# Optimization experiments

Measured on AMD Instinct MI355X. Metric: run time of the kernel, lower is better.

## Reference

```python
import jax, jax.numpy as jnp
import numpy as np

T_OUT = 12  # num_timesteps_output


def setup_inputs() -> dict:
    key = jax.random.key(0)
    ks = jax.random.split(key, 12)
    B, N, T, F = 32, 325, 12, 2
    C, H = 10, 64
    s = 0.08  # weight init scale (~1/sqrt(H)) to keep gates in sane range
    return {
        "A": jnp.zeros((N, N), jnp.float32),
        "X": jax.random.normal(ks[0], (B, N, T, F), jnp.float32),
        "enc_Wih": jax.random.normal(ks[1], (C, 3 * H, F), jnp.float32) * s,
        "enc_Whh": jax.random.normal(ks[2], (C, 3 * H, H), jnp.float32) * s,
        "enc_bih": jax.random.normal(ks[3], (C, 3 * H), jnp.float32) * s,
        "enc_bhh": jax.random.normal(ks[4], (C, 3 * H), jnp.float32) * s,
        "dec_Wih": jax.random.normal(ks[5], (C, 3 * H, 1), jnp.float32) * s,
        "dec_Whh": jax.random.normal(ks[6], (C, 3 * H, H), jnp.float32) * s,
        "dec_bih": jax.random.normal(ks[7], (C, 3 * H), jnp.float32) * s,
        "dec_bhh": jax.random.normal(ks[8], (C, 3 * H), jnp.float32) * s,
        "lin_W": jax.random.normal(ks[9], (C, 1, H), jnp.float32) * s,
        "lin_b": jax.random.normal(ks[10], (C, 1), jnp.float32) * s,
        "embed": jax.random.normal(ks[11], (N, C), jnp.float32),
    }


def _gru_update(gi, gh, h, H):
    # PyTorch GRU gate order: r, z, n
    r = jax.nn.sigmoid(gi[..., :H] + gh[..., :H])
    z = jax.nn.sigmoid(gi[..., H:2 * H] + gh[..., H:2 * H])
    n = jnp.tanh(gi[..., 2 * H:] + r * gh[..., 2 * H:])
    return (1.0 - z) * n + z * h


def reference(A, X, enc_Wih, enc_Whh, enc_bih, enc_bhh,
              dec_Wih, dec_Whh, dec_bih, dec_bhh, lin_W, lin_b, embed):
    B, N, T, F = X.shape
    C = enc_Wih.shape[0]
    H = enc_Whh.shape[-1]
    BN = B * N

    # (T, BN, F): time-major, batch*nodes flattened (matches X.view(-1,T,F).permute(1,0,2))
    Xs = jnp.transpose(X.reshape(BN, T, F), (1, 0, 2))

    def enc_step(h, x_t):  # h: (C, BN, H), x_t: (BN, F)
        gi = jnp.einsum('bf,cgf->cbg', x_t, enc_Wih) + enc_bih[:, None, :]
        gh = jnp.einsum('cbh,cgh->cbg', h, enc_Whh) + enc_bhh[:, None, :]
        return _gru_update(gi, gh, h, H), None

    h0 = jnp.zeros((C, BN, H), X.dtype)
    h_enc, _ = jax.lax.scan(enc_step, h0, Xs)  # (C, BN, H)

    # initial decoder input: last observed value of feature 0
    lv0 = jnp.broadcast_to(Xs[-1, :, 0][None, :, None], (C, BN, 1))

    def dec_step(carry, _):
        h, lv = carry
        gi = jnp.einsum('cbf,cgf->cbg', lv, dec_Wih) + dec_bih[:, None, :]
        gh = jnp.einsum('cbh,cgh->cbg', h, dec_Whh) + dec_bhh[:, None, :]
        h = _gru_update(gi, gh, h, H)
        value = jnp.einsum('cbh,coh->cbo', h, lin_W) + lin_b[:, None, :]  # (C, BN, 1)
        # original does last_value = value.detach()
        return (h, jax.lax.stop_gradient(value)), value

    (_, _), vals = jax.lax.scan(dec_step, (h_enc, lv0), None, length=T_OUT)
    # vals: (T_out, C, BN, 1) -> (B, N, T_out, C)
    out = jnp.transpose(vals[..., 0], (2, 0, 1)).reshape(B, N, T_OUT, C)

    weight = jax.nn.softmax(embed, axis=-1)  # (N, C)
    return jnp.einsum('bntc,nc->bnt', out, weight)
```

## Files before the change

### kernel.cpp

```cpp
#include <hip/hip_runtime.h>
#include <math.h>

#define N_     325
#define BN_    10400
#define OUTSZ_ (BN_*12)
#define RB_    208
#define WV_    13
#define THR_   832


typedef _Float16 h8v  __attribute__((ext_vector_type(8)));
typedef float    f4v  __attribute__((ext_vector_type(4)));
typedef unsigned int u32x4 __attribute__((ext_vector_type(4)));

#define L1C 1.4426950408889634f
#define L2C 2.8853900817779268f

__device__ __forceinline__ float rcp_f(float x){ return __builtin_amdgcn_rcpf(x); }
#if __has_builtin(__builtin_amdgcn_exp2f)
__device__ __forceinline__ float exp2_f(float x){ return __builtin_amdgcn_exp2f(x); }
#else
__device__ __forceinline__ float exp2_f(float x){ return __expf(x * 0.6931471805599453f); }
#endif

__device__ __forceinline__ unsigned short f16u(float x){
    union { _Float16 h; unsigned short u; } cv; cv.h = (_Float16)x; return cv.u;
}

#define BOFF   0
#define EOFF   24576
#define HOFF   27648
#define XOFF   57600
#define WOFF   67584
#define LOFF   68416
#define SMEMSZ 69248

#define MFMA(A,B,C) __builtin_amdgcn_mfma_f32_16x16x32_f16((A),(B),(C),0,0,0)

__device__ __forceinline__ void stage_main(const float* __restrict__ W, char* smem, int tid)
{
#pragma unroll
    for (int it = 0; it < 2; ++it) {
        int a16 = it*THR_ + tid;
        if (a16 < 1536) {
            int f     = a16 >> 6;
            int lanew = a16 & 63;
            int colf  = lanew & 15;
            int kb4   = lanew >> 4;
            int ch    = f & 1;
            int ct    = (f >> 1) & 3;
            int g     = f >> 3;
            int gc    = g*64 + ct*16 + colf;
            int k0    = ch*32 + kb4*8;
            float sc  = (g < 2) ? -L1C : -L2C;
            const float* p = W + gc*64 + k0;
            float4 a = *(const float4*)p;
            float4 b = *(const float4*)(p+4);
            h8v v;
            v[0]=(_Float16)(sc*a.x); v[1]=(_Float16)(sc*a.y);
            v[2]=(_Float16)(sc*a.z); v[3]=(_Float16)(sc*a.w);
            v[4]=(_Float16)(sc*b.x); v[5]=(_Float16)(sc*b.y);
            v[6]=(_Float16)(sc*b.z); v[7]=(_Float16)(sc*b.w);
            *(h8v*)(smem + BOFF + a16*16) = v;
        }
    }
}

__device__ __forceinline__ void rnn_step(h8v Aeh, h8v Ah0, h8v Ah1,
                                         const char* bb, const char* eb,
                                         const float cbh[4], float (&hreg)[4][4],
                                         char* wp)
{
    const f4v Z0 = {0.f,0.f,0.f,0.f};
#pragma unroll
    for (int ct = 0; ct < 4; ++ct) {
        f4v a0 = MFMA(Aeh, *(const h8v*)(eb + ct*256),       Z0);
        a0 = MFMA(Ah0, *(const h8v*)(bb + (ct*2   )*1024), a0);
        a0 = MFMA(Ah1, *(const h8v*)(bb + (ct*2+1 )*1024), a0);
        f4v a1 = MFMA(Aeh, *(const h8v*)(eb + (4+ct)*256),   Z0);
        a1 = MFMA(Ah0, *(const h8v*)(bb + (8+ct*2 )*1024), a1);
        a1 = MFMA(Ah1, *(const h8v*)(bb + (9+ct*2 )*1024), a1);
        f4v a3 = MFMA(Aeh, *(const h8v*)(eb + (8+ct)*256),   Z0);
        f4v a2 = MFMA(Ah0, *(const h8v*)(bb + (16+ct*2)*1024), Z0);
        a2 = MFMA(Ah1, *(const h8v*)(bb + (17+ct*2)*1024), a2);
#pragma unroll
        for (int i = 0; i < 4; ++i) {
            float er = exp2_f(a0[i]);
            float rr = rcp_f(1.0f + er);
            float ez = exp2_f(a1[i]);
            float en = exp2_f(fmaf(rr, a2[i] + cbh[ct], a3[i]));
            float h  = hreg[ct][i];
            float aa = 1.0f + ez;
            float den = fmaf(en, aa, aa);
            float t1  = fmaf(-en, ez, ez);
            float t2  = fmaf(en, h, h);
            float hnew = (t1 + t2) * rcp_f(den);
            hreg[ct][i] = hnew;
            *(_Float16*)(wp + i*144 + 32*ct) = (_Float16)hnew;
        }
    }
}

__global__ void __launch_bounds__(THR_, 6) krnn_kernel(
    const float* __restrict__ X,
    const float* __restrict__ eWih, const float* __restrict__ eWhh,
    const float* __restrict__ ebih, const float* __restrict__ ebhh,
    const float* __restrict__ dWih, const float* __restrict__ dWhh,
    const float* __restrict__ dbih, const float* __restrict__ dbhh,
    const float* __restrict__ linW, const float* __restrict__ linb,
    const float* __restrict__ embed, float* __restrict__ ws)
{
    __shared__ __align__(16) char smem[SMEMSZ];

    const int c    = blockIdx.y;
    const int row0 = blockIdx.x * RB_;
    const int tid  = threadIdx.x;
    const int lane = tid & 63;
    const int w    = tid >> 6;
    const int l15  = lane & 15;
    const int kg   = lane >> 4;

    stage_main(eWhh + c*12288, smem, tid);

    if (tid < 192) {
        int e = tid >> 4, ln = tid & 15;
        int g = e >> 2, ct = e & 3;
        int gc = g*64 + ct*16 + ln;
        float sc = (g < 2) ? -L1C : -L2C;
        float w0 = eWih[c*384 + gc*2], w1 = eWih[c*384 + gc*2 + 1];
        float bb_ = (g < 2) ? (ebih[c*192+gc] + ebhh[c*192+gc]) : ebih[c*192+gc];
        unsigned short* d = (unsigned short*)(smem + EOFF + e*256 + ln*16);
        d[0] = f16u(sc*w0); d[1] = f16u(sc*w1); d[2] = f16u(sc*bb_);
        d[3]=0; d[4]=0; d[5]=0; d[6]=0; d[7]=0;
    }
    for (int i = tid; i < RB_*12; i += THR_) {
        int r = i / 12, t = i - r*12;
        int rg = row0 + r;
        const float* p = X + (size_t)rg*24 + t*2;
        unsigned v = (unsigned)f16u(p[0]) | ((unsigned)f16u(p[1]) << 16);
        *(unsigned*)(smem + XOFF + r*48 + t*4) = v;
    }
    if (tid < RB_) {
        int r = row0 + tid;
        int n = r % N_;
        float e[10], mx = -1e30f;
#pragma unroll
        for (int cc=0; cc<10; ++cc){ e[cc]=embed[n*10+cc]; mx=fmaxf(mx,e[cc]); }
        float den = 0.0f;
#pragma unroll
        for (int cc=0; cc<10; ++cc) den += exp2_f((e[cc]-mx)*L1C);
        *(float*)(smem + WOFF + tid*4) = exp2_f((e[c]-mx)*L1C) * rcp_f(den);
    }
    for (int i = tid; i < WV_*576; i += THR_)
        *(unsigned*)(smem + HOFF + i*4) = 0u;

    float cbh[4];
#pragma unroll
    for (int ct=0; ct<4; ++ct) cbh[ct] = -L2C * ebhh[c*192 + 128 + l15 + 16*ct];

    __syncthreads();

    float wreg[4];
#pragma unroll
    for (int i=0;i<4;++i) wreg[i] = *(const float*)(smem + WOFF + (w*16 + kg*4 + i)*4);

    char* hp = smem + HOFF + w*2304;
    const int rdo = l15*144 + kg*16;
    char* wp = hp + kg*576 + l15*2;
    const char* bb = smem + lane*16;
    const char* eb = smem + EOFF + l15*16;

    float hreg[4][4];
#pragma unroll
    for (int ct=0; ct<4; ++ct)
#pragma unroll
        for (int i=0;i<4;++i) hreg[ct][i] = 0.0f;

    for (int t = 0; t < 12; ++t) {
        unsigned xd = *(const unsigned*)(smem + XOFF + (w*16 + l15)*48 + t*4);
        union { u32x4 u; h8v h; } ae;
        ae.u.x = (lane < 16) ? xd : 0u;
        ae.u.y = (lane < 16) ? 0x00003C00u : 0u;
        ae.u.z = 0u; ae.u.w = 0u;
        h8v Ah0 = *(const h8v*)(hp + rdo);
        h8v Ah1 = *(const h8v*)(hp + rdo + 64);
        rnn_step(ae.h, Ah0, Ah1, bb, eb, cbh, hreg, wp);
    }

    unsigned aew = (*(const unsigned*)(smem + XOFF + (w*16 + l15)*48 + 44) & 0xFFFFu)
                   | 0x3C000000u;

    __syncthreads();

    stage_main(dWhh + c*12288, smem, tid);
    if (tid < 192) {
        int e = tid >> 4, ln = tid & 15;
        int g = e >> 2, ct = e & 3;
        int gc = g*64 + ct*16 + ln;
        float k0, k1;
        if (g < 2) { k0 = -L1C*dWih[c*192+gc]; k1 = -L1C*(dbih[c*192+gc]+dbhh[c*192+gc]); }
        else       { k0 = -L2C*dWih[c*192+gc]; k1 = -L2C*dbih[c*192+gc]; }
        unsigned short* d = (unsigned short*)(smem + EOFF + e*256 + ln*16);
        d[0] = f16u(k0); d[1] = f16u(k1);
        d[2]=0; d[3]=0; d[4]=0; d[5]=0; d[6]=0; d[7]=0;
    }
    h8v Blw[2];
#pragma unroll
    for (int ch=0; ch<2; ++ch) {
        const float* p = linW + c*64 + ch*32 + kg*8;
        float4 a = *(const float4*)p;
        float4 b = *(const float4*)(p+4);
        h8v v;
        v[0]=(_Float16)a.x; v[1]=(_Float16)a.y; v[2]=(_Float16)a.z; v[3]=(_Float16)a.w;
        v[4]=(_Float16)b.x; v[5]=(_Float16)b.y; v[6]=(_Float16)b.z; v[7]=(_Float16)b.w;
        Blw[ch] = v;
    }
#pragma unroll
    for (int ct=0; ct<4; ++ct) cbh[ct] = -L2C * dbhh[c*192 + 128 + l15 + 16*ct];
    const float lb = linb[c];
    float* __restrict__ wsc = ws + (size_t)c * OUTSZ_;

    __syncthreads();

    for (int s = 0; s < 12; ++s) {
        h8v Ah0 = *(const h8v*)(hp + rdo);
        h8v Ah1 = *(const h8v*)(hp + rdo + 64);
        if (s > 0) {
            const f4v Zv = {0.f,0.f,0.f,0.f};
            f4v av = MFMA(Ah0, Blw[0], Zv);
            av = MFMA(Ah1, Blw[1], av);
            if (l15 == 0) {
#pragma unroll
                for (int i=0;i<4;++i) {
                    float lv = av[i] + lb;
                    *(float*)(smem + LOFF + w*64 + (kg*4+i)*4) = lv;
                    int r = row0 + w*16 + kg*4 + i;
                    wsc[(size_t)r*12 + (s-1)] = wreg[i]*lv;
                }
            }
            float lvme = *(const float*)(smem + LOFF + w*64 + l15*4);
            aew = (unsigned)f16u(lvme) | 0x3C000000u;
        }
        union { u32x4 u; h8v h; } ae;
        ae.u.x = (lane < 16) ? aew : 0u;
        ae.u.y = 0u; ae.u.z = 0u; ae.u.w = 0u;
        rnn_step(ae.h, Ah0, Ah1, bb, eb, cbh, hreg, wp);
    }

    {
        h8v Ah0 = *(const h8v*)(hp + rdo);
        h8v Ah1 = *(const h8v*)(hp + rdo + 64);
        const f4v Zv = {0.f,0.f,0.f,0.f};
        f4v av = MFMA(Ah0, Blw[0], Zv);
        av = MFMA(Ah1, Blw[1], av);
        if (l15 == 0) {
#pragma unroll
            for (int i=0;i<4;++i) {
                float lv = av[i] + lb;
                int r = row0 + w*16 + kg*4 + i;
                wsc[(size_t)r*12 + 11] = wreg[i]*lv;
            }
        }
    }
}

__global__ void __launch_bounds__(256) mix_kernel(const float* __restrict__ ws,
                                                  float* __restrict__ out)
{
    int i = blockIdx.x * 256 + threadIdx.x;
    if (i < OUTSZ_) {
        float s = 0.0f;
#pragma unroll
        for (int c = 0; c < 10; ++c) s += ws[(size_t)c * OUTSZ_ + i];
        out[i] = s;
    }
}

extern "C" void kernel_launch(void* const* d_in, const int* in_sizes, int n_in,
                              void* d_out, int out_size, void* d_ws, size_t ws_size,
                              hipStream_t stream) {
    const float* X    = (const float*)d_in[1];
    const float* eWih = (const float*)d_in[2];
    const float* eWhh = (const float*)d_in[3];
    const float* ebih = (const float*)d_in[4];
    const float* ebhh = (const float*)d_in[5];
    const float* dWih = (const float*)d_in[6];
    const float* dWhh = (const float*)d_in[7];
    const float* dbih = (const float*)d_in[8];
    const float* dbhh = (const float*)d_in[9];
    const float* linW = (const float*)d_in[10];
    const float* linb = (const float*)d_in[11];
    const float* emb  = (const float*)d_in[12];
    float* ws  = (float*)d_ws;
    float* out = (float*)d_out;

    dim3 grid(BN_ / RB_, 10);
    krnn_kernel<<<grid, dim3(THR_), 0, stream>>>(
        X, eWih, eWhh, ebih, ebhh, dWih, dWhh, dbih, dbhh, linW, linb, emb, ws);
    mix_kernel<<<(OUTSZ_ + 255) / 256, dim3(256), 0, stream>>>(ws, out);
}
```

Measured before the change: 228.6 us.

## Move decoder linear weights and softmax weights to LDS to cut registers

Stores the fp16 decoder output-projection weights in shared memory, and reads the per-row softmax mixing weights from shared memory at use instead of keeping both in registers. Adds a scheduling barrier after each gate tile in the RNN step and raises the launch-bounds occupancy hint from 6 to 8 waves. The aim is lower VGPR pressure so more waves fit or fewer registers spill. The cost is extra LDS reads inside the time loop, plus a scheduling barrier that may block instruction interleaving.

```diff
diff --git a/kernel.cpp b/kernel.cpp
--- a/kernel.cpp
+++ b/kernel.cpp
@@ -33,7 +33,8 @@
 #define XOFF   57600
 #define WOFF   67584
 #define LOFF   68416
-#define SMEMSZ 69248
+#define LWOFF  69248
+#define SMEMSZ 71296
 
 #define MFMA(A,B,C) __builtin_amdgcn_mfma_f32_16x16x32_f16((A),(B),(C),0,0,0)
 
@@ -98,10 +99,11 @@
             hreg[ct][i] = hnew;
             *(_Float16*)(wp + i*144 + 32*ct) = (_Float16)hnew;
         }
-    }
-}
-
-__global__ void __launch_bounds__(THR_, 6) krnn_kernel(
+        __builtin_amdgcn_sched_barrier(0);
+    }
+}
+
+__global__ void __launch_bounds__(THR_, 8) krnn_kernel(
     const float* __restrict__ X,
     const float* __restrict__ eWih, const float* __restrict__ eWhh,
     const float* __restrict__ ebih, const float* __restrict__ ebhh,
@@ -159,10 +161,6 @@
     for (int ct=0; ct<4; ++ct) cbh[ct] = -L2C * ebhh[c*192 + 128 + l15 + 16*ct];
 
     __syncthreads();
-
-    float wreg[4];
-#pragma unroll
-    for (int i=0;i<4;++i) wreg[i] = *(const float*)(smem + WOFF + (w*16 + kg*4 + i)*4);
 
     char* hp = smem + HOFF + w*2304;
     const int rdo = l15*144 + kg*16;
@@ -204,16 +202,12 @@
         d[0] = f16u(k0); d[1] = f16u(k1);
         d[2]=0; d[3]=0; d[4]=0; d[5]=0; d[6]=0; d[7]=0;
     }
-    h8v Blw[2];
-#pragma unroll
-    for (int ch=0; ch<2; ++ch) {
-        const float* p = linW + c*64 + ch*32 + kg*8;
-        float4 a = *(const float4*)p;
-        float4 b = *(const float4*)(p+4);
-        h8v v;
-        v[0]=(_Float16)a.x; v[1]=(_Float16)a.y; v[2]=(_Float16)a.z; v[3]=(_Float16)a.w;
-        v[4]=(_Float16)b.x; v[5]=(_Float16)b.y; v[6]=(_Float16)b.z; v[7]=(_Float16)b.w;
-        Blw[ch] = v;
+    if (tid < 128) {
+        int ch = tid >> 6, ln = tid & 63;
+        int kb = ch*32 + (ln >> 4)*8;
+        unsigned short* d = (unsigned short*)(smem + LWOFF + ch*1024 + ln*16);
+#pragma unroll
+        for (int j=0;j<8;++j) d[j] = f16u(linW[c*64 + kb + j]);
     }
 #pragma unroll
     for (int ct=0; ct<4; ++ct) cbh[ct] = -L2C * dbhh[c*192 + 128 + l15 + 16*ct];
@@ -227,15 +221,16 @@
         h8v Ah1 = *(const h8v*)(hp + rdo + 64);
         if (s > 0) {
             const f4v Zv = {0.f,0.f,0.f,0.f};
-            f4v av = MFMA(Ah0, Blw[0], Zv);
-            av = MFMA(Ah1, Blw[1], av);
+            f4v av = MFMA(Ah0, *(const h8v*)(smem + LWOFF + lane*16), Zv);
+            av = MFMA(Ah1, *(const h8v*)(smem + LWOFF + 1024 + lane*16), av);
             if (l15 == 0) {
 #pragma unroll
                 for (int i=0;i<4;++i) {
                     float lv = av[i] + lb;
                     *(float*)(smem + LOFF + w*64 + (kg*4+i)*4) = lv;
                     int r = row0 + w*16 + kg*4 + i;
-                    wsc[(size_t)r*12 + (s-1)] = wreg[i]*lv;
+                    float wg = *(const float*)(smem + WOFF + (w*16 + kg*4 + i)*4);
+                    wsc[(size_t)r*12 + (s-1)] = wg*lv;
                 }
             }
             float lvme = *(const float*)(smem + LOFF + w*64 + l15*4);
@@ -251,14 +246,15 @@
         h8v Ah0 = *(const h8v*)(hp + rdo);
         h8v Ah1 = *(const h8v*)(hp + rdo + 64);
         const f4v Zv = {0.f,0.f,0.f,0.f};
-        f4v av = MFMA(Ah0, Blw[0], Zv);
-        av = MFMA(Ah1, Blw[1], av);
+        f4v av = MFMA(Ah0, *(const h8v*)(smem + LWOFF + lane*16), Zv);
+        av = MFMA(Ah1, *(const h8v*)(smem + LWOFF + 1024 + lane*16), av);
         if (l15 == 0) {
 #pragma unroll
             for (int i=0;i<4;++i) {
                 float lv = av[i] + lb;
                 int r = row0 + w*16 + kg*4 + i;
-                wsc[(size_t)r*12 + 11] = wreg[i]*lv;
+                float wg = *(const float*)(smem + WOFF + (w*16 + kg*4 + i)*4);
+                wsc[(size_t)r*12 + 11] = wg*lv;
             }
         }
     }
```

Result: no change. 228.1 us (-0.2%).
